# Optimization experiments

Hardware: AMD Instinct MI355X
Metric: run time of the kernel (lower is better)

Reference implementation:

```python
import jax, jax.numpy as jnp
import numpy as np

EPS = 1e-5


def setup_inputs() -> dict:
    key = jax.random.key(0)
    ks = jax.random.split(key, 12)
    B, S, M, D, H, dh = 8, 512, 512, 1024, 16, 64
    T = S + M
    w_scale = 0.03  # keep attention logits in a sane range (mimics nn.Linear init scale)
    return {
        "x": jax.random.normal(ks[0], (B, S, D), jnp.float32),
        "mem": jax.random.normal(ks[1], (B, M, D), jnp.float32),
        "R": jax.random.normal(ks[2], (T, D), jnp.float32),
        "u": jax.random.normal(ks[3], (1, H, 1, dh), jnp.float32) * 0.1,
        "t": jax.random.normal(ks[4], (1, H, 1, dh), jnp.float32) * 0.1,
        "Wq": jax.random.normal(ks[5], (H * dh, D), jnp.float32) * w_scale,
        "Wk": jax.random.normal(ks[6], (H * dh, D), jnp.float32) * w_scale,
        "Wv": jax.random.normal(ks[7], (H * dh, D), jnp.float32) * w_scale,
        "Wr": jax.random.normal(ks[8], (H * dh, D), jnp.float32) * w_scale,
        "Wo": jax.random.normal(ks[9], (D, H * dh), jnp.float32) * w_scale,
        "gamma": jnp.ones((D,), jnp.float32),
        "beta": jnp.zeros((D,), jnp.float32),
    }


def reference(x, mem, R, u, t, Wq, Wk, Wv, Wr, Wo, gamma, beta):
    B, S, D = x.shape
    H, dh = u.shape[1], u.shape[3]
    h = jnp.concatenate([mem, x], axis=1)          # [B, T, D]
    T = h.shape[1]
    M = T - S

    q = (x @ Wq.T).reshape(B, S, H, dh).transpose(0, 2, 1, 3)   # [B,H,S,dh]
    k = (h @ Wk.T).reshape(B, T, H, dh).transpose(0, 2, 1, 3)   # [B,H,T,dh]
    v = (h @ Wv.T).reshape(B, T, H, dh).transpose(0, 2, 1, 3)   # [B,H,T,dh]
    r = (R[-T:] @ Wr.T).reshape(1, T, H, dh).transpose(0, 2, 1, 3)  # [1,H,T,dh]

    ac = jnp.einsum("bhid,bhjd->bhij", q + u, k)                # [B,H,S,T]
    bd = jnp.einsum("bhid,hjd->bhij", q + t, r[0])              # [B,H,S,T]

    # circulant shift: shifted[..., i, j] = bd[..., i, (j - i + S - 1) % T]
    idx = (jnp.arange(T)[None, :] - jnp.arange(S)[:, None] + S - 1) % T  # [S,T]
    bd = jnp.take_along_axis(bd, idx[None, None], axis=3)

    # causal mask with memory offset: keep j <= i + M (tril(mem_len)), then
    # exact-zero entries (the masked ones) become -inf, matching the original.
    mask = jnp.arange(T)[None, :] <= (jnp.arange(S)[:, None] + M)        # [S,T]
    score = jnp.where(mask[None, None], (ac + bd) / jnp.sqrt(jnp.float32(dh)), 0.0)
    score = jnp.where(score == 0, -jnp.inf, score)
    p = jax.nn.softmax(score, axis=-1)                                   # [B,H,S,T]

    att = jnp.einsum("bhij,bhjd->bhid", p, v).transpose(0, 2, 1, 3).reshape(B, S, H * dh)
    out = att @ Wo.T                                                      # dropout is identity (p=0/eval)

    y = out + x
    mu = jnp.mean(y, axis=-1, keepdims=True)
    var = jnp.var(y, axis=-1, keepdims=True)
    return (y - mu) / jnp.sqrt(var + EPS) * gamma + beta
```

## Files before the change

kernel.cpp:

```cpp
#include <hip/hip_runtime.h>
#include <math.h>

#define BB 8
#define SS 512
#define MM 512
#define TT 1024
#define DD 1024
#define HH 16
#define DH 64

typedef __attribute__((ext_vector_type(8))) short bf16x8;
typedef __attribute__((ext_vector_type(4))) float f32x4;

#define SCL2E 0.1803368801111f
#define DTHR 11.5f

__device__ __forceinline__ ushort f2bf(float f) {
  union { float f; unsigned u; } x; x.f = f;
  unsigned r = x.u + 0x7fffu + ((x.u >> 16) & 1u);
  return (ushort)(r >> 16);
}
__device__ __forceinline__ float bf2f(ushort u) {
  return __builtin_bit_cast(float, ((unsigned)u) << 16);
}

__device__ __forceinline__ void stage16(void* lds, const void* g) {
  __builtin_amdgcn_global_load_lds((const __attribute__((address_space(1))) void*)g,
                                   (__attribute__((address_space(3))) void*)lds, 16, 0, 0);
}

template <int C>
__device__ __forceinline__ float dppf(float x) {
  return __builtin_bit_cast(float,
      __builtin_amdgcn_update_dpp(0, __builtin_bit_cast(int, x), C, 0xF, 0xF, true));
}
__device__ __forceinline__ float redmax16(float x) {
  x = fmaxf(x, dppf<0xB1>(x));
  x = fmaxf(x, dppf<0x4E>(x));
  x = fmaxf(x, dppf<0x141>(x));
  x = fmaxf(x, dppf<0x140>(x));
  return x;
}
__device__ __forceinline__ float redsum16(float x) {
  x += dppf<0xB1>(x);
  x += dppf<0x4E>(x);
  x += dppf<0x141>(x);
  x += dppf<0x140>(x);
  return x;
}
__device__ __forceinline__ float bperm_f(int byteaddr, float v) {
  return __builtin_bit_cast(float,
      __builtin_amdgcn_ds_bpermute(byteaddr, __builtin_bit_cast(int, v)));
}

__global__ __launch_bounds__(256) void cast_all(
    const float* __restrict__ mem, const float* __restrict__ x,
    const float* __restrict__ R, const float* __restrict__ Wq,
    const float* __restrict__ Wk, const float* __restrict__ Wv,
    const float* __restrict__ Wr, const float* __restrict__ Wo,
    ushort* __restrict__ hb, ushort* __restrict__ Rb, ushort* __restrict__ Wqb,
    ushort* __restrict__ Wkb, ushort* __restrict__ Wvb, ushort* __restrict__ Wrb,
    ushort* __restrict__ Wob) {
  const int M1 = 1 << 20;
  int i = (blockIdx.x * 256 + threadIdx.x) * 8;
  const float* src;
  ushort* dst;
  if (i < 4 * M1) {
    src = mem + i;
    dst = hb + (size_t)i + (size_t)(i >> 19) * 524288;
  } else if (i < 8 * M1) {
    int j = i - 4 * M1;
    src = x + j;
    dst = hb + (size_t)j + (size_t)(j >> 19) * 524288 + 524288;
  } else if (i < 9 * M1) {
    src = R + (i - 8 * M1);  dst = Rb + (i - 8 * M1);
  } else if (i < 10 * M1) {
    src = Wq + (i - 9 * M1); dst = Wqb + (i - 9 * M1);
  } else if (i < 11 * M1) {
    src = Wk + (i - 10 * M1); dst = Wkb + (i - 10 * M1);
  } else if (i < 12 * M1) {
    src = Wv + (i - 11 * M1); dst = Wvb + (i - 11 * M1);
  } else if (i < 13 * M1) {
    src = Wr + (i - 12 * M1); dst = Wrb + (i - 12 * M1);
  } else {
    src = Wo + (i - 13 * M1); dst = Wob + (i - 13 * M1);
  }
  float4 a = *(const float4*)(src);
  float4 c = *(const float4*)(src + 4);
  union { bf16x8 v; ushort u[8]; } pk;
  pk.u[0] = f2bf(a.x); pk.u[1] = f2bf(a.y); pk.u[2] = f2bf(a.z); pk.u[3] = f2bf(a.w);
  pk.u[4] = f2bf(c.x); pk.u[5] = f2bf(c.y); pk.u[6] = f2bf(c.z); pk.u[7] = f2bf(c.w);
  *(bf16x8*)(void*)dst = pk.v;
}

__global__ __launch_bounds__(256) void gemm_qkvr(
    const ushort* __restrict__ hb, const ushort* __restrict__ Rbuf,
    const ushort* __restrict__ Wqb, const ushort* __restrict__ Wkb,
    const ushort* __restrict__ Wvb, const ushort* __restrict__ Wrb,
    ushort* __restrict__ qub, ushort* __restrict__ qtb,
    ushort* __restrict__ kbo, ushort* __restrict__ vtb, ushort* __restrict__ rbo,
    const float* __restrict__ uvec, const float* __restrict__ tvec) {
  __shared__ ushort As[128 * 32];
  __shared__ ushort Bs[128 * 32];
  const int bid = (blockIdx.x & 7) * 168 + (blockIdx.x >> 3);
  const ushort* A;
  const ushort* W;
  ushort* C0 = nullptr;
  ushort* C1 = nullptr;
  bool dual = false, qslice = false, vmode = false;
  int mt, nx;
  if (bid < 256) {
    int r = bid; mt = r >> 3; nx = r & 7;
    A = hb; W = Wqb; C0 = qub; C1 = qtb; dual = true; qslice = true;
  } else if (bid < 768) {
    int r = bid - 256; mt = r >> 3; nx = r & 7;
    A = hb; W = Wkb; C0 = kbo;
  } else if (bid < 1280) {
    int r = bid - 768; mt = r >> 3; nx = r & 7;
    A = hb; W = Wvb; C0 = vtb; vmode = true;
  } else {
    int r = bid - 1280; mt = r >> 3; nx = r & 7;
    A = Rbuf; W = Wrb; C0 = rbo;
  }
  const int m0 = mt * 128, n0 = nx * 128;

  const int t = threadIdx.x;
  const int w = t >> 6, l = t & 63;
  const int m16 = l & 15, kg = l >> 4;
  const int wr = w >> 1, wc = w & 1;

  const int c0 = t, c1 = t + 256;
  const int scol = (((t & 3) ^ ((t >> 3) & 3)) * 8);
  const ushort* asrc0;
  const ushort* asrc1;
  {
    int gm0 = m0 + (c0 >> 2), gm1 = m0 + (c1 >> 2);
    if (qslice) {
      asrc0 = A + ((size_t)((gm0 >> 9) * TT + MM + (gm0 & 511))) * DD + scol;
      asrc1 = A + ((size_t)((gm1 >> 9) * TT + MM + (gm1 & 511))) * DD + scol;
    } else {
      asrc0 = A + (size_t)gm0 * DD + scol;
      asrc1 = A + (size_t)gm1 * DD + scol;
    }
  }
  const ushort* bsrc0 = W + (size_t)(n0 + (c0 >> 2)) * DD + scol;
  const ushort* bsrc1 = W + (size_t)(n0 + (c1 >> 2)) * DD + scol;
  ushort* adst0 = As + c0 * 8;
  ushort* adst1 = As + c1 * 8;
  ushort* bdst0 = Bs + c0 * 8;
  ushort* bdst1 = Bs + c1 * 8;

  const int cbx = ((kg ^ ((m16 >> 1) & 3)) << 3);

  f32x4 acc[4][4];
#pragma unroll
  for (int mi = 0; mi < 4; ++mi)
#pragma unroll
    for (int ni = 0; ni < 4; ++ni) acc[mi][ni] = (f32x4){0.f, 0.f, 0.f, 0.f};

  for (int k0 = 0; k0 < DD; k0 += 32) {
    stage16(adst0, asrc0 + k0);
    stage16(adst1, asrc1 + k0);
    stage16(bdst0, bsrc0 + k0);
    stage16(bdst1, bsrc1 + k0);
    __syncthreads();
    bf16x8 af[4], bfr[4];
#pragma unroll
    for (int mi = 0; mi < 4; ++mi)
      af[mi] = *(const bf16x8*)(const void*)&As[(wr * 64 + mi * 16 + m16) * 32 + cbx];
#pragma unroll
    for (int ni = 0; ni < 4; ++ni)
      bfr[ni] = *(const bf16x8*)(const void*)&Bs[(wc * 64 + ni * 16 + m16) * 32 + cbx];
#pragma unroll
    for (int mi = 0; mi < 4; ++mi)
#pragma unroll
      for (int ni = 0; ni < 4; ++ni)
        acc[mi][ni] = __builtin_amdgcn_mfma_f32_16x16x32_bf16(af[mi], bfr[ni], acc[mi][ni], 0, 0, 0);
    __syncthreads();
  }

  const int rbase = m0 + wr * 64 + kg * 4;
  const int cbase = n0 + wc * 64 + m16;
  if (vmode) {
    const int bb = m0 >> 10;
    const int tt0 = (m0 & 1023) + wr * 64 + kg * 4;
#pragma unroll
    for (int mi = 0; mi < 4; ++mi)
#pragma unroll
      for (int ni = 0; ni < 4; ++ni) {
        ushort4 o;
        o.x = f2bf(acc[mi][ni][0]); o.y = f2bf(acc[mi][ni][1]);
        o.z = f2bf(acc[mi][ni][2]); o.w = f2bf(acc[mi][ni][3]);
        *(ushort4*)(C0 + ((size_t)(bb * 1024 + cbase + ni * 16) << 10) + tt0 + mi * 16) = o;
      }
  } else if (dual) {
    float uv[4], tv[4];
#pragma unroll
    for (int ni = 0; ni < 4; ++ni) { uv[ni] = uvec[cbase + ni * 16]; tv[ni] = tvec[cbase + ni * 16]; }
#pragma unroll
    for (int mi = 0; mi < 4; ++mi)
#pragma unroll
      for (int ni = 0; ni < 4; ++ni)
#pragma unroll
        for (int rg = 0; rg < 4; ++rg) {
          size_t idx = (size_t)(rbase + mi * 16 + rg) * DD + cbase + ni * 16;
          C0[idx] = f2bf(acc[mi][ni][rg] + uv[ni]);
          C1[idx] = f2bf(acc[mi][ni][rg] + tv[ni]);
        }
  } else {
#pragma unroll
    for (int mi = 0; mi < 4; ++mi)
#pragma unroll
      for (int ni = 0; ni < 4; ++ni)
#pragma unroll
        for (int rg = 0; rg < 4; ++rg)
          C0[(size_t)(rbase + mi * 16 + rg) * DD + cbase + ni * 16] = f2bf(acc[mi][ni][rg]);
  }
}

__global__ __launch_bounds__(256) void gemm_wo(const ushort* __restrict__ A,
                                               const ushort* __restrict__ W,
                                               ushort* __restrict__ Cb) {
  __shared__ ushort As[128 * 32];
  __shared__ ushort Bs[128 * 32];
  const int bid = (blockIdx.x & 7) * 32 + (blockIdx.x >> 3);
  const int mt = bid >> 3, nx = bid & 7;
  const int m0 = mt * 128, n0 = nx * 128;
  const int t = threadIdx.x;
  const int w = t >> 6, l = t & 63;
  const int m16 = l & 15, kg = l >> 4;
  const int wr = w >> 1, wc = w & 1;

  const int c0 = t, c1 = t + 256;
  const int scol = (((t & 3) ^ ((t >> 3) & 3)) * 8);
  const ushort* asrc0 = A + (size_t)(m0 + (c0 >> 2)) * DD + scol;
  const ushort* asrc1 = A + (size_t)(m0 + (c1 >> 2)) * DD + scol;
  const ushort* bsrc0 = W + (size_t)(n0 + (c0 >> 2)) * DD + scol;
  const ushort* bsrc1 = W + (size_t)(n0 + (c1 >> 2)) * DD + scol;
  ushort* adst0 = As + c0 * 8;
  ushort* adst1 = As + c1 * 8;
  ushort* bdst0 = Bs + c0 * 8;
  ushort* bdst1 = Bs + c1 * 8;

  const int cbx = ((kg ^ ((m16 >> 1) & 3)) << 3);

  f32x4 acc[4][4];
#pragma unroll
  for (int mi = 0; mi < 4; ++mi)
#pragma unroll
    for (int ni = 0; ni < 4; ++ni) acc[mi][ni] = (f32x4){0.f, 0.f, 0.f, 0.f};

  for (int k0 = 0; k0 < DD; k0 += 32) {
    stage16(adst0, asrc0 + k0);
    stage16(adst1, asrc1 + k0);
    stage16(bdst0, bsrc0 + k0);
    stage16(bdst1, bsrc1 + k0);
    __syncthreads();
    bf16x8 af[4], bfr[4];
#pragma unroll
    for (int mi = 0; mi < 4; ++mi)
      af[mi] = *(const bf16x8*)(const void*)&As[(wr * 64 + mi * 16 + m16) * 32 + cbx];
#pragma unroll
    for (int ni = 0; ni < 4; ++ni)
      bfr[ni] = *(const bf16x8*)(const void*)&Bs[(wc * 64 + ni * 16 + m16) * 32 + cbx];
#pragma unroll
    for (int mi = 0; mi < 4; ++mi)
#pragma unroll
      for (int ni = 0; ni < 4; ++ni)
        acc[mi][ni] = __builtin_amdgcn_mfma_f32_16x16x32_bf16(af[mi], bfr[ni], acc[mi][ni], 0, 0, 0);
    __syncthreads();
  }

  const int rbase = m0 + wr * 64 + kg * 4;
  const int cbase = n0 + wc * 64 + m16;
#pragma unroll
  for (int mi = 0; mi < 4; ++mi)
#pragma unroll
    for (int ni = 0; ni < 4; ++ni)
#pragma unroll
      for (int rg = 0; rg < 4; ++rg)
        Cb[(size_t)(rbase + mi * 16 + rg) * DD + cbase + ni * 16] = f2bf(acc[mi][ni][rg]);
}

__global__ __launch_bounds__(256) void attn_mfma(const ushort* __restrict__ qu,
                                                 const ushort* __restrict__ qt,
                                                 const ushort* __restrict__ kb,
                                                 const ushort* __restrict__ vt,
                                                 const ushort* __restrict__ rb,
                                                 ushort* __restrict__ att) {
  const int w = threadIdx.x >> 6;
  const int l = threadIdx.x & 63;
  const int m16 = l & 15;
  const int kg = l >> 4;
  const int bid = blockIdx.x;
  const int it = 7 - (bid >> 7);
  const int bh = bid & 127;
  const int b = bh >> 4, h = bh & 15;
  const int i0 = it * 64;

  __shared__ ushort Ks[2][4096];
  __shared__ ushort Vs[4096];
  __shared__ ushort Rl[8192];
  __shared__ ushort plds[4][16][72];

  bf16x8 aqu[2], aqt[2];
  {
    const ushort* qrow = qu + ((size_t)(b * SS + i0 + w * 16 + m16)) * DD + h * DH + kg * 8;
    aqu[0] = *(const bf16x8*)(const void*)(qrow);
    aqu[1] = *(const bf16x8*)(const void*)(qrow + 32);
    const ushort* qrow2 = qt + ((size_t)(b * SS + i0 + w * 16 + m16)) * DD + h * DH + kg * 8;
    aqt[0] = *(const bf16x8*)(const void*)(qrow2);
    aqt[1] = *(const bf16x8*)(const void*)(qrow2 + 32);
  }

  int baddr[4];
  bool bsel[4];
#pragma unroll
  for (int rg = 0; rg < 4; ++rg) {
    const int rw = kg * 4 + rg;
    baddr[rg] = (kg * 16 + ((m16 + 15 - rw) & 15)) << 2;
    bsel[rg] = m16 > rw;
  }

  const int c0 = threadIdx.x, c1 = threadIdx.x + 256;
  const int r0 = c0 >> 3, sc0 = ((c0 & 7) * 8) ^ ((r0 & 7) << 3);
  const int r1 = c1 >> 3, sc1 = ((c1 & 7) * 8) ^ ((r1 & 7) << 3);
  const ushort* kp0 = kb + ((size_t)(b * TT) + r0) * DD + h * DH + sc0;
  const ushort* kp1 = kb + ((size_t)(b * TT) + r1) * DD + h * DH + sc1;
  const ushort* vp0 = vt + ((size_t)(b * 1024 + h * DH + r0)) * 1024 + sc0;
  const ushort* vp1 = vt + ((size_t)(b * 1024 + h * DH + r1)) * 1024 + sc1;

  const int cb0 = (kg * 8) ^ ((m16 & 7) << 3);
  const int cb1 = (kg * 8 + 32) ^ ((m16 & 7) << 3);
  int slot64[5];
#pragma unroll
  for (int f = 0; f < 5; ++f)
    slot64[f] = ((496 - i0 - w * 16 + m16 + f * 16) & 127) << 6;

  {
    const int base0 = 448 - i0;
#pragma unroll
    for (int kk = 0; kk < 4; ++kk) {
      int c = threadIdx.x + kk * 256;
      int ro = c >> 3, cc = c & 7;
      int p = base0 + ro;
      int slot = p & 127;
      stage16(Rl + slot * 64 + cc * 8,
              rb + (size_t)p * DD + h * DH + ((cc * 8) ^ ((ro & 7) << 3)));
    }
  }
  stage16(&Ks[0][c0 * 8], kp0);
  stage16(&Ks[0][c1 * 8], kp1);
  stage16(Vs + c0 * 8, vp0);
  stage16(Vs + c1 * 8, vp1);
  kp0 += (size_t)64 * DD; kp1 += (size_t)64 * DD;
  vp0 += 64; vp1 += 64;

  f32x4 O[4];
  float mrow[4], lrow[4];
#pragma unroll
  for (int nt = 0; nt < 4; ++nt) O[nt] = (f32x4){0.f, 0.f, 0.f, 0.f};
#pragma unroll
  for (int rg = 0; rg < 4; ++rg) { mrow[rg] = -1e30f; lrow[rg] = 0.f; }

  const int ntj = it + 9;
  int cur = 0;
  for (int jt = 0; jt < ntj; ++jt) {
    const int j0 = jt * 64;

    if (jt > 0) {
      stage16(Vs + c0 * 8, vp0);
      stage16(Vs + c1 * 8, vp1);
      vp0 += 64; vp1 += 64;
      const int pstart = 512 + j0 - i0;
#pragma unroll
      for (int kk = 0; kk < 2; ++kk) {
        int c = threadIdx.x + kk * 256;
        int ro = c >> 3, cc = c & 7;
        int p = pstart + ro;
        int pc = p < 1023 ? p : 1023;
        int slot = p & 127;
        stage16(Rl + slot * 64 + cc * 8,
                rb + (size_t)pc * DD + h * DH + ((cc * 8) ^ ((ro & 7) << 3)));
      }
    }
    __syncthreads();

    const ushort* kbase = &Ks[cur][0];
    f32x4 ac[4];
    __builtin_amdgcn_s_setprio(1);
#pragma unroll
    for (int nt = 0; nt < 4; ++nt) {
      ac[nt] = (f32x4){0.f, 0.f, 0.f, 0.f};
      const int row = nt * 16 + m16;
#pragma unroll
      for (int ks = 0; ks < 2; ++ks) {
        bf16x8 bk = *(const bf16x8*)(const void*)(kbase + row * 64 + (ks == 0 ? cb0 : cb1));
        ac[nt] = __builtin_amdgcn_mfma_f32_16x16x32_bf16(aqu[ks], bk, ac[nt], 0, 0, 0);
      }
    }
    __builtin_amdgcn_s_setprio(0);

    if (jt + 1 < ntj) {
      stage16(&Ks[cur ^ 1][c0 * 8], kp0);
      stage16(&Ks[cur ^ 1][c1 * 8], kp1);
      kp0 += (size_t)64 * DD; kp1 += (size_t)64 * DD;
    }

    f32x4 bd[5];
    __builtin_amdgcn_s_setprio(1);
#pragma unroll
    for (int f = 0; f < 5; ++f) {
      f32x4 z = (f32x4){0.f, 0.f, 0.f, 0.f};
      bf16x8 b0 = *(const bf16x8*)(const void*)(Rl + slot64[f] + cb0);
      z = __builtin_amdgcn_mfma_f32_16x16x32_bf16(aqt[0], b0, z, 0, 0, 0);
      bf16x8 b1 = *(const bf16x8*)(const void*)(Rl + slot64[f] + cb1);
      bd[f] = __builtin_amdgcn_mfma_f32_16x16x32_bf16(aqt[1], b1, z, 0, 0, 0);
    }
    __builtin_amdgcn_s_setprio(0);
#pragma unroll
    for (int f = 0; f < 5; ++f) slot64[f] = (slot64[f] + 4096) & 8191;

    float sca[4][4];
#pragma unroll
    for (int rg = 0; rg < 4; ++rg) {
      float rr[5];
#pragma unroll
      for (int f = 0; f < 5; ++f) rr[f] = bperm_f(baddr[rg], bd[f][rg]);
#pragma unroll
      for (int nt = 0; nt < 4; ++nt) {
        float bdv = bsel[rg] ? rr[nt + 1] : rr[nt];
        sca[nt][rg] = (ac[nt][rg] + bdv) * SCL2E;
      }
    }
    if (jt == ntj - 1) {
#pragma unroll
      for (int rg = 0; rg < 4; ++rg) {
        const int jmax = i0 + w * 16 + kg * 4 + rg + MM;
#pragma unroll
        for (int nt = 0; nt < 4; ++nt)
          sca[nt][rg] = (j0 + nt * 16 + m16 <= jmax) ? sca[nt][rg] : -1e30f;
      }
    }

    float pmax[4];
#pragma unroll
    for (int rg = 0; rg < 4; ++rg) {
      float pm = fmaxf(fmaxf(sca[0][rg], sca[1][rg]), fmaxf(sca[2][rg], sca[3][rg]));
      pmax[rg] = redmax16(pm);
    }
    bool grow = false;
#pragma unroll
    for (int rg = 0; rg < 4; ++rg) grow = grow || (pmax[rg] > mrow[rg] + DTHR);
    if (__any(grow)) {
#pragma unroll
      for (int rg = 0; rg < 4; ++rg) {
        float mnew = fmaxf(mrow[rg], pmax[rg]);
        float scale = __builtin_amdgcn_exp2f(mrow[rg] - mnew);
        mrow[rg] = mnew;
        lrow[rg] *= scale;
#pragma unroll
        for (int nt = 0; nt < 4; ++nt) O[nt][rg] *= scale;
      }
    }

#pragma unroll
    for (int rg = 0; rg < 4; ++rg) {
      float ps = 0.f;
#pragma unroll
      for (int nt = 0; nt < 4; ++nt) {
        float p = __builtin_amdgcn_exp2f(sca[nt][rg] - mrow[rg]);
        ps += p;
        plds[w][kg * 4 + rg][nt * 16 + m16] = f2bf(p);
      }
      lrow[rg] += redsum16(ps);
    }

    __builtin_amdgcn_s_setprio(1);
#pragma unroll
    for (int ks = 0; ks < 2; ++ks) {
      bf16x8 pa = *(const bf16x8*)(const void*)&plds[w][m16][kg * 8 + ks * 32];
#pragma unroll
      for (int nt = 0; nt < 4; ++nt) {
        bf16x8 vf = *(const bf16x8*)(const void*)(Vs + (nt * 16 + m16) * 64 + (ks == 0 ? cb0 : cb1));
        O[nt] = __builtin_amdgcn_mfma_f32_16x16x32_bf16(pa, vf, O[nt], 0, 0, 0);
      }
    }
    __builtin_amdgcn_s_setprio(0);

    __syncthreads();
    cur ^= 1;
  }

  float linv[4];
#pragma unroll
  for (int rg = 0; rg < 4; ++rg) linv[rg] = 1.f / lrow[rg];
#pragma unroll
  for (int nt = 0; nt < 4; ++nt) {
#pragma unroll
    for (int rg = 0; rg < 4; ++rg) {
      att[((size_t)(b * SS + i0 + w * 16 + kg * 4 + rg)) * DD + h * DH + nt * 16 + m16] =
          f2bf(O[nt][rg] * linv[rg]);
    }
  }
}

__global__ __launch_bounds__(256) void ln_kernel(const ushort* __restrict__ ypre,
                                                 const float* __restrict__ x,
                                                 const float* __restrict__ gamma,
                                                 const float* __restrict__ beta,
                                                 float* __restrict__ out) {
  const int row = blockIdx.x;
  const int t = threadIdx.x;
  const int lane = t & 63, w = t >> 6;
  const ushort* yr = ypre + (size_t)row * DD;
  const float* xr = x + (size_t)row * DD;

  ushort4 yv = *(const ushort4*)(yr + t * 4);
  float4 xv = *(const float4*)(xr + t * 4);
  float v0 = bf2f(yv.x) + xv.x, v1 = bf2f(yv.y) + xv.y;
  float v2 = bf2f(yv.z) + xv.z, v3 = bf2f(yv.w) + xv.w;

  float s = v0 + v1 + v2 + v3;
  float ss = v0 * v0 + v1 * v1 + v2 * v2 + v3 * v3;
  __shared__ float rs[4], rss[4];
#pragma unroll
  for (int off = 32; off; off >>= 1) {
    s += __shfl_xor(s, off);
    ss += __shfl_xor(ss, off);
  }
  if (!lane) { rs[w] = s; rss[w] = ss; }
  __syncthreads();
  s = rs[0] + rs[1] + rs[2] + rs[3];
  ss = rss[0] + rss[1] + rss[2] + rss[3];
  const float mu = s * (1.f / DD);
  const float var = ss * (1.f / DD) - mu * mu;
  const float rstd = rsqrtf(var + 1e-5f);

  float4 g = *(const float4*)(gamma + t * 4);
  float4 be = *(const float4*)(beta + t * 4);
  float4 o;
  o.x = (v0 - mu) * rstd * g.x + be.x;
  o.y = (v1 - mu) * rstd * g.y + be.y;
  o.z = (v2 - mu) * rstd * g.z + be.z;
  o.w = (v3 - mu) * rstd * g.w + be.w;
  *(float4*)(out + (size_t)row * DD + t * 4) = o;
}

extern "C" void kernel_launch(void* const* d_in, const int* in_sizes, int n_in,
                              void* d_out, int out_size, void* d_ws, size_t ws_size,
                              hipStream_t stream) {
  const float* x = (const float*)d_in[0];
  const float* mem = (const float*)d_in[1];
  const float* R = (const float*)d_in[2];
  const float* u = (const float*)d_in[3];
  const float* tv = (const float*)d_in[4];
  const float* Wq = (const float*)d_in[5];
  const float* Wk = (const float*)d_in[6];
  const float* Wv = (const float*)d_in[7];
  const float* Wr = (const float*)d_in[8];
  const float* Wo = (const float*)d_in[9];
  const float* gamma = (const float*)d_in[10];
  const float* beta = (const float*)d_in[11];
  float* out = (float*)d_out;

  ushort* hb = (ushort*)d_ws;
  ushort* Rb = hb + (8u << 20);
  ushort* Wqb = Rb + (1u << 20);
  ushort* Wkb = Wqb + (1u << 20);
  ushort* Wvb = Wkb + (1u << 20);
  ushort* Wrb = Wvb + (1u << 20);
  ushort* Wob = Wrb + (1u << 20);
  ushort* qu_b = Wob + (1u << 20);
  ushort* qt_b = qu_b + (4u << 20);
  ushort* kb = qt_b + (4u << 20);
  ushort* vt = kb + (8u << 20);
  ushort* rb = vt + (8u << 20);
  ushort* att = qu_b;
  ushort* ypre = kb;

  dim3 blk(256);

  cast_all<<<dim3(7168), blk, 0, stream>>>(mem, x, R, Wq, Wk, Wv, Wr, Wo,
                                           hb, Rb, Wqb, Wkb, Wvb, Wrb, Wob);

  gemm_qkvr<<<dim3(1344), blk, 0, stream>>>(hb, Rb, Wqb, Wkb, Wvb, Wrb,
                                            qu_b, qt_b, kb, vt, rb, u, tv);

  attn_mfma<<<dim3(BB * HH * 8), blk, 0, stream>>>(qu_b, qt_b, kb, vt, rb, att);

  gemm_wo<<<dim3(256), blk, 0, stream>>>(att, Wob, ypre);

  ln_kernel<<<dim3(BB * SS), blk, 0, stream>>>(ypre, x, gamma, beta, out);
}
```

Measured before the change: 178.6 us.

## Drop q+t buffer, derive it in attention; retile Wo GEMM; read bf16 residual

```diff
diff --git a/kernel.cpp b/kernel.cpp
--- a/kernel.cpp
+++ b/kernel.cpp
@@ -97,21 +97,20 @@
     const ushort* __restrict__ hb, const ushort* __restrict__ Rbuf,
     const ushort* __restrict__ Wqb, const ushort* __restrict__ Wkb,
     const ushort* __restrict__ Wvb, const ushort* __restrict__ Wrb,
-    ushort* __restrict__ qub, ushort* __restrict__ qtb,
+    ushort* __restrict__ qub,
     ushort* __restrict__ kbo, ushort* __restrict__ vtb, ushort* __restrict__ rbo,
-    const float* __restrict__ uvec, const float* __restrict__ tvec) {
+    const float* __restrict__ uvec) {
   __shared__ ushort As[128 * 32];
   __shared__ ushort Bs[128 * 32];
   const int bid = (blockIdx.x & 7) * 168 + (blockIdx.x >> 3);
   const ushort* A;
   const ushort* W;
   ushort* C0 = nullptr;
-  ushort* C1 = nullptr;
-  bool dual = false, qslice = false, vmode = false;
+  bool qadd = false, qslice = false, vmode = false;
   int mt, nx;
   if (bid < 256) {
     int r = bid; mt = r >> 3; nx = r & 7;
-    A = hb; W = Wqb; C0 = qub; C1 = qtb; dual = true; qslice = true;
+    A = hb; W = Wqb; C0 = qub; qadd = true; qslice = true;
   } else if (bid < 768) {
     int r = bid - 256; mt = r >> 3; nx = r & 7;
     A = hb; W = Wkb; C0 = kbo;
@@ -193,20 +192,17 @@
         o.z = f2bf(acc[mi][ni][2]); o.w = f2bf(acc[mi][ni][3]);
         *(ushort4*)(C0 + ((size_t)(bb * 1024 + cbase + ni * 16) << 10) + tt0 + mi * 16) = o;
       }
-  } else if (dual) {
-    float uv[4], tv[4];
-#pragma unroll
-    for (int ni = 0; ni < 4; ++ni) { uv[ni] = uvec[cbase + ni * 16]; tv[ni] = tvec[cbase + ni * 16]; }
+  } else if (qadd) {
+    float uv[4];
+#pragma unroll
+    for (int ni = 0; ni < 4; ++ni) uv[ni] = uvec[cbase + ni * 16];
 #pragma unroll
     for (int mi = 0; mi < 4; ++mi)
 #pragma unroll
       for (int ni = 0; ni < 4; ++ni)
 #pragma unroll
-        for (int rg = 0; rg < 4; ++rg) {
-          size_t idx = (size_t)(rbase + mi * 16 + rg) * DD + cbase + ni * 16;
-          C0[idx] = f2bf(acc[mi][ni][rg] + uv[ni]);
-          C1[idx] = f2bf(acc[mi][ni][rg] + tv[ni]);
-        }
+        for (int rg = 0; rg < 4; ++rg)
+          C0[(size_t)(rbase + mi * 16 + rg) * DD + cbase + ni * 16] = f2bf(acc[mi][ni][rg] + uv[ni]);
   } else {
 #pragma unroll
     for (int mi = 0; mi < 4; ++mi)
@@ -222,71 +218,68 @@
                                                const ushort* __restrict__ W,
                                                ushort* __restrict__ Cb) {
   __shared__ ushort As[128 * 32];
-  __shared__ ushort Bs[128 * 32];
-  const int bid = (blockIdx.x & 7) * 32 + (blockIdx.x >> 3);
-  const int mt = bid >> 3, nx = bid & 7;
-  const int m0 = mt * 128, n0 = nx * 128;
+  __shared__ ushort Bs[64 * 32];
+  const int bid = (blockIdx.x & 7) * 64 + (blockIdx.x >> 3);
+  const int mt = bid >> 4, nxt = bid & 15;
+  const int m0 = mt * 128, n0 = nxt * 64;
   const int t = threadIdx.x;
   const int w = t >> 6, l = t & 63;
   const int m16 = l & 15, kg = l >> 4;
   const int wr = w >> 1, wc = w & 1;
 
-  const int c0 = t, c1 = t + 256;
   const int scol = (((t & 3) ^ ((t >> 3) & 3)) * 8);
-  const ushort* asrc0 = A + (size_t)(m0 + (c0 >> 2)) * DD + scol;
-  const ushort* asrc1 = A + (size_t)(m0 + (c1 >> 2)) * DD + scol;
-  const ushort* bsrc0 = W + (size_t)(n0 + (c0 >> 2)) * DD + scol;
-  const ushort* bsrc1 = W + (size_t)(n0 + (c1 >> 2)) * DD + scol;
-  ushort* adst0 = As + c0 * 8;
-  ushort* adst1 = As + c1 * 8;
-  ushort* bdst0 = Bs + c0 * 8;
-  ushort* bdst1 = Bs + c1 * 8;
+  const ushort* asrc0 = A + (size_t)(m0 + (t >> 2)) * DD + scol;
+  const ushort* asrc1 = A + (size_t)(m0 + 64 + (t >> 2)) * DD + scol;
+  const ushort* bsrc0 = W + (size_t)(n0 + (t >> 2)) * DD + scol;
+  ushort* adst0 = As + t * 8;
+  ushort* adst1 = As + (t + 256) * 8;
+  ushort* bdst0 = Bs + t * 8;
 
   const int cbx = ((kg ^ ((m16 >> 1) & 3)) << 3);
 
-  f32x4 acc[4][4];
+  f32x4 acc[4][2];
 #pragma unroll
   for (int mi = 0; mi < 4; ++mi)
 #pragma unroll
-    for (int ni = 0; ni < 4; ++ni) acc[mi][ni] = (f32x4){0.f, 0.f, 0.f, 0.f};
+    for (int ni = 0; ni < 2; ++ni) acc[mi][ni] = (f32x4){0.f, 0.f, 0.f, 0.f};
 
   for (int k0 = 0; k0 < DD; k0 += 32) {
     stage16(adst0, asrc0 + k0);
     stage16(adst1, asrc1 + k0);
     stage16(bdst0, bsrc0 + k0);
-    stage16(bdst1, bsrc1 + k0);
     __syncthreads();
-    bf16x8 af[4], bfr[4];
+    bf16x8 af[4], bfr[2];
 #pragma unroll
     for (int mi = 0; mi < 4; ++mi)
       af[mi] = *(const bf16x8*)(const void*)&As[(wr * 64 + mi * 16 + m16) * 32 + cbx];
 #pragma unroll
-    for (int ni = 0; ni < 4; ++ni)
-      bfr[ni] = *(const bf16x8*)(const void*)&Bs[(wc * 64 + ni * 16 + m16) * 32 + cbx];
-#pragma unroll
-    for (int mi = 0; mi < 4; ++mi)
-#pragma unroll
-      for (int ni = 0; ni < 4; ++ni)
+    for (int ni = 0; ni < 2; ++ni)
+      bfr[ni] = *(const bf16x8*)(const void*)&Bs[(wc * 32 + ni * 16 + m16) * 32 + cbx];
+#pragma unroll
+    for (int mi = 0; mi < 4; ++mi)
+#pragma unroll
+      for (int ni = 0; ni < 2; ++ni)
         acc[mi][ni] = __builtin_amdgcn_mfma_f32_16x16x32_bf16(af[mi], bfr[ni], acc[mi][ni], 0, 0, 0);
     __syncthreads();
   }
 
   const int rbase = m0 + wr * 64 + kg * 4;
-  const int cbase = n0 + wc * 64 + m16;
+  const int cbase = n0 + wc * 32 + m16;
 #pragma unroll
   for (int mi = 0; mi < 4; ++mi)
 #pragma unroll
-    for (int ni = 0; ni < 4; ++ni)
+    for (int ni = 0; ni < 2; ++ni)
 #pragma unroll
       for (int rg = 0; rg < 4; ++rg)
         Cb[(size_t)(rbase + mi * 16 + rg) * DD + cbase + ni * 16] = f2bf(acc[mi][ni][rg]);
 }
 
 __global__ __launch_bounds__(256) void attn_mfma(const ushort* __restrict__ qu,
-                                                 const ushort* __restrict__ qt,
                                                  const ushort* __restrict__ kb,
                                                  const ushort* __restrict__ vt,
                                                  const ushort* __restrict__ rb,
+                                                 const float* __restrict__ uvec,
+                                                 const float* __restrict__ tvec,
                                                  ushort* __restrict__ att) {
   const int w = threadIdx.x >> 6;
   const int l = threadIdx.x & 63;
@@ -308,9 +301,16 @@
     const ushort* qrow = qu + ((size_t)(b * SS + i0 + w * 16 + m16)) * DD + h * DH + kg * 8;
     aqu[0] = *(const bf16x8*)(const void*)(qrow);
     aqu[1] = *(const bf16x8*)(const void*)(qrow + 32);
-    const ushort* qrow2 = qt + ((size_t)(b * SS + i0 + w * 16 + m16)) * DD + h * DH + kg * 8;
-    aqt[0] = *(const bf16x8*)(const void*)(qrow2);
-    aqt[1] = *(const bf16x8*)(const void*)(qrow2 + 32);
+#pragma unroll
+    for (int ks = 0; ks < 2; ++ks) {
+      ushort* a = (ushort*)&aqt[ks];
+      const ushort* qa = (const ushort*)&aqu[ks];
+#pragma unroll
+      for (int e = 0; e < 8; ++e) {
+        const int col = h * DH + kg * 8 + ks * 32 + e;
+        a[e] = f2bf(bf2f(qa[e]) + (tvec[col] - uvec[col]));
+      }
+    }
   }
 
   int baddr[4];
@@ -506,7 +506,7 @@
 }
 
 __global__ __launch_bounds__(256) void ln_kernel(const ushort* __restrict__ ypre,
-                                                 const float* __restrict__ x,
+                                                 const ushort* __restrict__ hb,
                                                  const float* __restrict__ gamma,
                                                  const float* __restrict__ beta,
                                                  float* __restrict__ out) {
@@ -514,12 +514,12 @@
   const int t = threadIdx.x;
   const int lane = t & 63, w = t >> 6;
   const ushort* yr = ypre + (size_t)row * DD;
-  const float* xr = x + (size_t)row * DD;
+  const ushort* xr = hb + ((size_t)((row >> 9) * TT + MM + (row & 511))) * DD;
 
   ushort4 yv = *(const ushort4*)(yr + t * 4);
-  float4 xv = *(const float4*)(xr + t * 4);
-  float v0 = bf2f(yv.x) + xv.x, v1 = bf2f(yv.y) + xv.y;
-  float v2 = bf2f(yv.z) + xv.z, v3 = bf2f(yv.w) + xv.w;
+  ushort4 xv = *(const ushort4*)(xr + t * 4);
+  float v0 = bf2f(yv.x) + bf2f(xv.x), v1 = bf2f(yv.y) + bf2f(xv.y);
+  float v2 = bf2f(yv.z) + bf2f(xv.z), v3 = bf2f(yv.w) + bf2f(xv.w);
 
   float s = v0 + v1 + v2 + v3;
   float ss = v0 * v0 + v1 * v1 + v2 * v2 + v3 * v3;
@@ -572,8 +572,7 @@
   ushort* Wrb = Wvb + (1u << 20);
   ushort* Wob = Wrb + (1u << 20);
   ushort* qu_b = Wob + (1u << 20);
-  ushort* qt_b = qu_b + (4u << 20);
-  ushort* kb = qt_b + (4u << 20);
+  ushort* kb = qu_b + (4u << 20);
   ushort* vt = kb + (8u << 20);
   ushort* rb = vt + (8u << 20);
   ushort* att = qu_b;
@@ -585,11 +584,11 @@
                                            hb, Rb, Wqb, Wkb, Wvb, Wrb, Wob);
 
   gemm_qkvr<<<dim3(1344), blk, 0, stream>>>(hb, Rb, Wqb, Wkb, Wvb, Wrb,
-                                            qu_b, qt_b, kb, vt, rb, u, tv);
-
-  attn_mfma<<<dim3(BB * HH * 8), blk, 0, stream>>>(qu_b, qt_b, kb, vt, rb, att);
-
-  gemm_wo<<<dim3(256), blk, 0, stream>>>(att, Wob, ypre);
-
-  ln_kernel<<<dim3(BB * SS), blk, 0, stream>>>(ypre, x, gamma, beta, out);
-}
+                                            qu_b, kb, vt, rb, u);
+
+  attn_mfma<<<dim3(BB * HH * 8), blk, 0, stream>>>(qu_b, kb, vt, rb, u, tv, att);
+
+  gemm_wo<<<dim3(512), blk, 0, stream>>>(att, Wob, ypre);
+
+  ln_kernel<<<dim3(BB * SS), blk, 0, stream>>>(ypre, hb, gamma, beta, out);
+}
```

Result: faster. 172.4 us (-3.5%).
